# Kernel optimization log

Hardware: AMD Instinct MI355X
Metric: run time of the kernel (lower is better)

## Reference

```python
import jax, jax.numpy as jnp
import numpy as np

N, E, B, L = 65536, 262144, 512, 1000
IN_DIM, HID, VOCAB = 74, 128, 25
CHANNELS = [HID, 96, 128, IN_DIM, HID]  # protein conv1d filter chain


def _conv1d(x, k):
    # x: [B, C_in, L], k: [C_out, C_in, 3], stride 1, padding 1 (like nn.Conv1d)
    return jax.lax.conv_general_dilated(x, k, (1,), ((1, 1),),
                                        dimension_numbers=('NCH', 'OIH', 'NCH'))


def setup_inputs() -> dict:
    key = jax.random.key(0)
    ks = jax.random.split(key, 20)

    def gl(k, shape, fan_in):
        return jax.random.normal(k, shape, jnp.float32) / np.float32(np.sqrt(fan_in))

    inp = {}
    inp['node_feats'] = jax.random.normal(ks[0], (N, IN_DIM), jnp.float32)
    # GraphConv (conv1): weight [in, hid]
    inp['W_gc'] = gl(ks[1], (IN_DIM, HID), IN_DIM)
    inp['b_gc'] = jnp.zeros((HID,), jnp.float32)
    # MLPNodeReadout: two linears (no activation between, per dgllife default)
    inp['W_ro_in'] = gl(ks[2], (HID, HID), HID)
    inp['b_ro_in'] = jnp.zeros((HID,), jnp.float32)
    inp['W_ro_out'] = gl(ks[3], (HID, HID), HID)
    inp['b_ro_out'] = jnp.zeros((HID,), jnp.float32)
    inp['Wc1'] = gl(ks[4], (HID, HID), HID); inp['bc1'] = jnp.zeros((HID,), jnp.float32)
    inp['Wc2'] = gl(ks[5], (HID, HID), HID); inp['bc2'] = jnp.zeros((HID,), jnp.float32)
    # protein embedding + 4 conv1d layers
    inp['embed'] = jax.random.normal(ks[6], (VOCAB, HID), jnp.float32)
    for i in range(4):
        cin, cout = CHANNELS[i], CHANNELS[i + 1]
        inp['K%d' % (i + 1)] = gl(ks[7 + i], (cout, cin, 3), cin * 3)
        inp['cb%d' % (i + 1)] = jnp.zeros((cout,), jnp.float32)
    # CPI head: Linear(2h,2h)+ReLU, Linear(2h,1)+Sigmoid
    inp['Wf1'] = gl(ks[11], (2 * HID, 2 * HID), 2 * HID); inp['bf1'] = jnp.zeros((2 * HID,), jnp.float32)
    inp['Wf2'] = gl(ks[12], (2 * HID, 1), 2 * HID); inp['bf2'] = jnp.zeros((1,), jnp.float32)
    # graph structure / protein tokens
    inp['edge_src'] = jax.random.randint(ks[13], (E,), 0, N, jnp.int32)
    inp['edge_dst'] = jax.random.randint(ks[14], (E,), 0, N, jnp.int32)
    inp['graph_ids'] = jnp.sort(jax.random.randint(ks[15], (N,), 0, B, jnp.int32))
    inp['protein_seq'] = jax.random.randint(ks[16], (B, L), 0, VOCAB, jnp.int32)
    return inp


def reference(node_feats, W_gc, b_gc, W_ro_in, b_ro_in, W_ro_out, b_ro_out,
              Wc1, bc1, Wc2, bc2, embed, K1, cb1, K2, cb2, K3, cb3, K4, cb4,
              Wf1, bf1, Wf2, bf2, edge_src, edge_dst, graph_ids, protein_seq):
    n = node_feats.shape[0]
    nb = protein_seq.shape[0]
    # dgl.add_self_loop: append self edges
    loop = jnp.arange(n, dtype=edge_src.dtype)
    src = jnp.concatenate([edge_src, loop])
    dst = jnp.concatenate([edge_dst, loop])
    ones = jnp.ones(src.shape[0], jnp.float32)
    deg_out = jax.ops.segment_sum(ones, src, n)  # out-degree (src norm)
    deg_in = jax.ops.segment_sum(ones, dst, n)   # in-degree (dst norm)
    h = node_feats * jax.lax.rsqrt(deg_out)[:, None]
    h = jax.ops.segment_sum(h[src], dst, n) * jax.lax.rsqrt(deg_in)[:, None]
    h = jax.nn.relu(h @ W_gc + b_gc)
    # MLPNodeReadout (sum over nodes per graph), then outer ReLU
    x = (h @ W_ro_in + b_ro_in) @ W_ro_out + b_ro_out
    hg = jax.nn.relu(jax.ops.segment_sum(x, graph_ids, nb))  # [B, HID]
    # compound FC layers (dropout = identity)
    cv = jax.nn.relu(hg @ Wc1 + bc1)
    cv = jax.nn.relu(cv @ Wc2 + bc2)
    pv = jnp.transpose(embed[protein_seq], (0, 2, 1))
    for K, b in ((K1, cb1), (K2, cb2), (K3, cb3), (K4, cb4)):
        pv = jax.nn.relu(_conv1d(pv, K) + b[None, :, None])
    pmax = jnp.max(pv, axis=-1)  # adaptive_max_pool1d(output_size=1) + squeeze
    # CPI head
    z = jnp.concatenate([cv, pmax], axis=1)  # [B, 2*HID]
    z = jax.nn.relu(z @ Wf1 + bf1)
    return jax.nn.sigmoid(z @ Wf2 + bf2)  # [B, 1]
```

## Files before the change

kernel.cpp:

```cpp
#include <hip/hip_runtime.h>
#include <math.h>

#define IN_DIM 74
#define HID 128
#define LSEQ 1000
#define RSA 272
#define RSB 208
#define TILE 50
#define R0 58
#define R1 56
#define R2 54
#define R3 52
#define NCHUNK 42
#define NGRP 14
#define WBUF_SZ 24576
#define LDS_BIAS 49152
#define LDS_ACT  50944
#define ACTA_SZ  15776
#define ACTB_SZ  11648
#define ACTB_BASE (LDS_ACT + 4*ACTA_SZ)
#define LDS_TOTAL (ACTB_BASE + 4*ACTB_SZ)

typedef unsigned int u32;
typedef unsigned short u16;

typedef __attribute__((ext_vector_type(8))) short bf16x8;
typedef __attribute__((ext_vector_type(4))) float f32x4;

__device__ __forceinline__ u16 f2bf(float f){
  u32 u = __float_as_uint(f);
  u32 r = (u + 0x7fffu + ((u >> 16) & 1u)) >> 16;
  return (u16)r;
}
__device__ __forceinline__ u32 pack2(float x, float y){
  return (u32)f2bf(x) | ((u32)f2bf(y) << 16);
}

__global__ void k_cnt_edge(const int* __restrict__ src, const int* __restrict__ dst,
                           int* out_cnt, int* in_cnt, int E){
  int e = blockIdx.x*256 + threadIdx.x;
  if (e < E){ atomicAdd(&out_cnt[src[e]], 1); atomicAdd(&in_cnt[dst[e]], 1); }
}
__global__ void k_scan1(const int* __restrict__ cnt, int* pref, int* bsum, int N){
  __shared__ int buf[256];
  int t = threadIdx.x, i = blockIdx.x*256 + t;
  int v = (i < N) ? cnt[i] : 0;
  buf[t] = v; __syncthreads();
  for (int o = 1; o < 256; o <<= 1){
    int tv = (t >= o) ? buf[t-o] : 0;
    __syncthreads(); buf[t] += tv; __syncthreads();
  }
  if (i < N) pref[i] = buf[t] - v;
  if (t == 255) bsum[blockIdx.x] = buf[255];
}
__global__ void k_scan2(int* bsum, int nb){
  __shared__ int buf[1024];
  int t = threadIdx.x;
  int v = (t < nb) ? bsum[t] : 0;
  buf[t] = v; __syncthreads();
  for (int o = 1; o < 1024; o <<= 1){
    int tv = (t >= o) ? buf[t-o] : 0;
    __syncthreads(); buf[t] += tv; __syncthreads();
  }
  if (t < nb) bsum[t] = buf[t] - v;
}
__global__ void k_scan3(const int* __restrict__ pref, const int* __restrict__ bsum,
                        int* offs, int* cur, int N){
  int i = blockIdx.x*256 + threadIdx.x;
  if (i < N){ int o = pref[i] + bsum[blockIdx.x]; offs[i] = o; cur[i] = o; }
}
__global__ void k_csr_fill(const int* __restrict__ src, const int* __restrict__ dst,
                           int* cur, int* csr_src, int E){
  int e = blockIdx.x*256 + threadIdx.x;
  if (e < E){ int slot = atomicAdd(&cur[dst[e]], 1); csr_src[slot] = src[e]; }
}
__global__ __launch_bounds__(256) void k_gather(const float* __restrict__ nf,
    const int* __restrict__ csr_src, const int* __restrict__ offs,
    const int* __restrict__ in_cnt, const int* __restrict__ out_cnt,
    float* __restrict__ h_agg, int N){
  int wid = threadIdx.x >> 6, lane = threadIdx.x & 63;
  int d = blockIdx.x*4 + wid;
  if (d >= N) return;
  int beg = offs[d], num = in_cnt[d];
  const float* row = nf + (size_t)d*IN_DIM;
  float ws = rsqrtf((float)out_cnt[d] + 1.f);
  float a0 = row[lane]*ws, a1 = 0.f;
  if (lane < IN_DIM-64) a1 = row[64+lane]*ws;
  for (int j = 0; j < num; ++j){
    int s = csr_src[beg + j];
    float w = rsqrtf((float)out_cnt[s] + 1.f);
    const float* rs = nf + (size_t)s*IN_DIM;
    a0 += rs[lane]*w;
    if (lane < IN_DIM-64) a1 += rs[64+lane]*w;
  }
  float sc = rsqrtf((float)num + 1.f);
  float* hp = h_agg + (size_t)d*IN_DIM;
  hp[lane] = a0*sc;
  if (lane < IN_DIM-64) hp[64+lane] = a1*sc;
}
__global__ __launch_bounds__(256) void k_gc_gemm(const float* __restrict__ h_agg,
        const float* __restrict__ W, const float* __restrict__ bias,
        float* __restrict__ h, int N){
  __shared__ float Wl[IN_DIM*HID];
  __shared__ float rowsT[IN_DIM][36];
  int base = blockIdx.x * 32;
  for (int idx = threadIdx.x; idx < IN_DIM*HID; idx += 256) Wl[idx] = W[idx];
  for (int idx = threadIdx.x; idx < 32*IN_DIM; idx += 256){
    int r = idx / IN_DIM, k = idx - r*IN_DIM;
    rowsT[k][r] = (base + r < N) ? h_agg[(size_t)(base+r)*IN_DIM + k] : 0.f;
  }
  __syncthreads();
  int c = threadIdx.x & 127, rh = threadIdx.x >> 7;
  float acc[16];
  #pragma unroll
  for (int i = 0; i < 16; ++i) acc[i] = 0.f;
  for (int k = 0; k < IN_DIM; ++k){
    float w = Wl[k*HID + c];
    const float4* rp = (const float4*)&rowsT[k][rh*16];
    float4 r0 = rp[0], r1 = rp[1], r2 = rp[2], r3 = rp[3];
    acc[0] += r0.x*w; acc[1] += r0.y*w; acc[2] += r0.z*w; acc[3] += r0.w*w;
    acc[4] += r1.x*w; acc[5] += r1.y*w; acc[6] += r1.z*w; acc[7] += r1.w*w;
    acc[8] += r2.x*w; acc[9] += r2.y*w; acc[10] += r2.z*w; acc[11] += r2.w*w;
    acc[12] += r3.x*w; acc[13] += r3.y*w; acc[14] += r3.z*w; acc[15] += r3.w*w;
  }
  float bv = bias[c];
  #pragma unroll
  for (int i = 0; i < 16; ++i){
    int r = base + rh*16 + i;
    if (r < N) h[(size_t)r*HID + c] = fmaxf(acc[i] + bv, 0.f);
  }
}
__global__ __launch_bounds__(128) void k_graph_tail(const float* __restrict__ h,
    const int* __restrict__ gid,
    const float* __restrict__ W_ri, const float* __restrict__ b_ri,
    const float* __restrict__ W_ro, const float* __restrict__ b_ro,
    const float* __restrict__ Wc1, const float* __restrict__ bc1,
    const float* __restrict__ Wc2, const float* __restrict__ bc2,
    float* __restrict__ z, int N){
  __shared__ float va[128], vb[128];
  __shared__ int bounds[2];
  int g = blockIdx.x, c = threadIdx.x;
  if (c < 2){
    int target = g + c, lo = 0, hi = N;
    while (lo < hi){ int mid = (lo+hi)>>1; if (gid[mid] < target) lo = mid+1; else hi = mid; }
    bounds[c] = lo;
  }
  __syncthreads();
  int lo = bounds[0], hi = bounds[1];
  float s = 0.f;
  for (int i = lo; i < hi; ++i) s += h[(size_t)i*HID + c];
  va[c] = s;
  float cn = (float)(hi - lo);
  __syncthreads();
  s = 0.f;
  for (int k = 0; k < 128; ++k) s += va[k]*W_ri[k*128 + c];
  vb[c] = s + b_ri[c]*cn;
  __syncthreads();
  s = 0.f;
  for (int k = 0; k < 128; ++k) s += vb[k]*W_ro[k*128 + c];
  va[c] = fmaxf(s + b_ro[c]*cn, 0.f);
  __syncthreads();
  s = 0.f;
  for (int k = 0; k < 128; ++k) s += va[k]*Wc1[k*128 + c];
  vb[c] = fmaxf(s + bc1[c], 0.f);
  __syncthreads();
  s = 0.f;
  for (int k = 0; k < 128; ++k) s += vb[k]*Wc2[k*128 + c];
  z[(size_t)g*256 + c] = fmaxf(s + bc2[c], 0.f);
}

__global__ void k_setup(const float* __restrict__ K1, const float* __restrict__ K2,
                        const float* __restrict__ K3, const float* __restrict__ K4,
                        const float* __restrict__ cb1, const float* __restrict__ cb2,
                        const float* __restrict__ cb3, const float* __restrict__ cb4,
                        u16* __restrict__ AW, float* __restrict__ ball,
                        float* __restrict__ z, int* __restrict__ out_cnt,
                        int* __restrict__ in_cnt, int N, int B){
  int idx = blockIdx.x*256 + threadIdx.x;
  if (idx < NCHUNK*4096){
    int g = idx >> 12, rem = idx & 4095;
    int co = rem >> 5, kk = rem & 31;
    const float* Kw; int CIN, CPAD, COUT, ksl;
    if (g < 12)      { Kw = K1; CIN = 128; CPAD = 128; COUT =  96; ksl = g; }
    else if (g < 21) { Kw = K2; CIN =  96; CPAD =  96; COUT = 128; ksl = g-12; }
    else if (g < 33) { Kw = K3; CIN =  74; CPAD = 128; COUT =  74; ksl = g-21; }
    else             { Kw = K4; CIN =  74; CPAD =  96; COUT = 128; ksl = g-33; }
    int k = ksl*32 + kk;
    int t = k / CPAD, ci = k - t*CPAD;
    float v = (co < COUT && ci < CIN) ? Kw[((size_t)co*CIN + ci)*3 + t] : 0.f;
    int sl2 = (kk >> 3) ^ ((co >> 1) & 3);
    AW[(size_t)g*4096 + co*32 + sl2*8 + (kk & 7)] = f2bf(v);
    return;
  }
  idx -= NCHUNK*4096;
  if (idx < 448){
    float v = 0.f;
    if (idx < 96) v = cb1[idx];
    else if (idx < 224) v = cb2[idx-96];
    else if (idx < 320){ int c = idx-224; v = (c < 74) ? cb3[c] : 0.f; }
    else v = cb4[idx-320];
    ball[idx] = v;
    return;
  }
  idx -= 448;
  if (idx < B*128){ z[(size_t)(idx>>7)*256 + 128 + (idx&127)] = 0.f; return; }
  idx -= B*128;
  if (idx < 2*N){
    if (idx < N) out_cnt[idx] = 0; else in_cnt[idx-N] = 0;
  }
}

__device__ __forceinline__ void stage24k(char* lds, int tid, const u16* src, int pbuf){
  const char* s = (const char*)src;
  char* d = lds + pbuf*WBUF_SZ;
  #pragma unroll
  for (int i = 0; i < 3; ++i)
    __builtin_amdgcn_global_load_lds(
      (const __attribute__((address_space(1))) unsigned*)(s + i*8192 + tid*16),
      (__attribute__((address_space(3))) unsigned*)(d + i*8192 + tid*16), 16, 0, 0);
}

template<int KS, int G0, int M, int TPC, int RS_IN, int RCAP>
__device__ __forceinline__ void conv_phases(char* lds, const char* actIn,
    const u16* __restrict__ AW, int co0, int lm, int cg, int scg, int tid,
    f32x4 (&acc)[M][4])
{
  #pragma unroll
  for (int m = 0; m < M; ++m)
    #pragma unroll
    for (int n = 0; n < 4; ++n) acc[m][n] = (f32x4){0.f,0.f,0.f,0.f};
  #pragma unroll
  for (int ks = 0; ks < KS; ++ks){
    const int g = G0 + ks;
    const char* wb = lds + ((g/3)&1)*WBUF_SZ + (g%3)*8192;
    bf16x8 Af[M];
    #pragma unroll
    for (int m = 0; m < M; ++m)
      Af[m] = *(const bf16x8*)(wb + (co0 + m*16 + lm)*64 + scg*16);
    const int tap = ks / TPC;
    const int c16 = (ks - tap*TPC)*4 + cg;
    bf16x8 Bf[4];
    #pragma unroll
    for (int n = 0; n < 4; ++n){
      int raw = n*16 + lm + tap;
      int row = raw < RCAP ? raw : RCAP;
      Bf[n] = *(const bf16x8*)(actIn + row*RS_IN + c16*16);
    }
    __builtin_amdgcn_s_setprio(1);
    #pragma unroll
    for (int m = 0; m < M; ++m)
      #pragma unroll
      for (int n = 0; n < 4; ++n)
        acc[m][n] = __builtin_amdgcn_mfma_f32_16x16x32_bf16(Af[m], Bf[n], acc[m][n], 0, 0, 0);
    __builtin_amdgcn_s_setprio(0);
    if ((g % 3) == 2 && (ks + 1 < KS)){
      __syncthreads();
      const int gn = g/3 + 2;
      if (gn < NGRP) stage24k(lds, tid, AW + (size_t)gn*12288, gn & 1);
    }
  }
}

template<int M>
__device__ __forceinline__ void epi_store(char* actOut, int RS_OUT,
    const float* lbias, int boff, int co0, int lm, int cg,
    int lbase, int nrows, f32x4 (&acc)[M][4])
{
  #pragma unroll
  for (int m = 0; m < M; ++m){
    int co = co0 + m*16 + cg*4;
    float4 bb = *(const float4*)(lbias + boff + co);
    #pragma unroll
    for (int n = 0; n < 4; ++n){
      int r1 = n*16 + lm;
      if (r1 < nrows){
        int l = lbase + r1;
        u32 lo = 0, hi = 0;
        if ((unsigned)l < (unsigned)LSEQ){
          f32x4 a = acc[m][n];
          lo = pack2(fmaxf(a[0]+bb.x, 0.f), fmaxf(a[1]+bb.y, 0.f));
          hi = pack2(fmaxf(a[2]+bb.z, 0.f), fmaxf(a[3]+bb.w, 0.f));
        }
        uint2 st; st.x = lo; st.y = hi;
        *(uint2*)(actOut + r1*RS_OUT + co*2) = st;
      }
    }
  }
}

__device__ __forceinline__ void epi_pool(const float* lbias, int boff,
    int co0, int lm, int cg, int l0, float* __restrict__ z, int b, f32x4 (&acc)[4][4])
{
  float mxv[4][4];
  #pragma unroll
  for (int m = 0; m < 4; ++m)
    #pragma unroll
    for (int j = 0; j < 4; ++j) mxv[m][j] = 0.f;
  #pragma unroll
  for (int m = 0; m < 4; ++m){
    float4 bb = *(const float4*)(lbias + boff + co0 + m*16 + cg*4);
    const float* bv = (const float*)&bb;
    #pragma unroll
    for (int n = 0; n < 4; ++n){
      int r1 = n*16 + lm;
      int l = l0 + r1;
      if (r1 < TILE && l < LSEQ){
        #pragma unroll
        for (int j = 0; j < 4; ++j)
          mxv[m][j] = fmaxf(mxv[m][j], fmaxf(acc[m][n][j] + bv[j], 0.f));
      }
    }
  }
  #pragma unroll
  for (int o = 1; o <= 8; o <<= 1)
    #pragma unroll
    for (int m = 0; m < 4; ++m)
      #pragma unroll
      for (int j = 0; j < 4; ++j)
        mxv[m][j] = fmaxf(mxv[m][j], __shfl_xor(mxv[m][j], o));
  if (lm == 0){
    float* zrow = z + (size_t)b*256 + 128;
    #pragma unroll
    for (int m = 0; m < 4; ++m)
      #pragma unroll
      for (int j = 0; j < 4; ++j)
        atomicMax((u32*)(zrow + co0 + m*16 + cg*4 + j), __float_as_uint(mxv[m][j]));
  }
}

__global__ __launch_bounds__(512, 1) void k_protein(
    const int* __restrict__ seq, const float* __restrict__ emb,
    const u16* __restrict__ AW, const float* __restrict__ ball,
    float* __restrict__ z)
{
  __shared__ __align__(16) char lds[LDS_TOTAL];
  const int tid = threadIdx.x;
  const int lane = tid & 63, wid = tid >> 6;
  const int lm = lane & 15, cg = lane >> 4;
  const int scg = cg ^ ((lm >> 1) & 3);
  const int tl = wid >> 1;
  const int h  = wid & 1;
  const int b  = blockIdx.y;
  const int l0 = (blockIdx.x*4 + tl) * TILE;

  for (int i = tid; i < 448; i += 512) ((float*)(lds + LDS_BIAS))[i] = ball[i];

  for (int idx = tid; idx < 4*R0*16; idx += 512){
    int t2 = idx / (R0*16), rem = idx - t2*(R0*16);
    int r = rem >> 4, p = rem & 15;
    int ll0 = (blockIdx.x*4 + t2) * TILE;
    int l = ll0 - 4 + r;
    uint4 st = make_uint4(0u,0u,0u,0u);
    if ((unsigned)l < (unsigned)LSEQ){
      int tok = seq[b*LSEQ + l];
      const float4* e = (const float4*)(emb + (size_t)tok*HID + p*8);
      float4 v0 = e[0], v1 = e[1];
      st.x = pack2(v0.x, v0.y); st.y = pack2(v0.z, v0.w);
      st.z = pack2(v1.x, v1.y); st.w = pack2(v1.z, v1.w);
    }
    *(uint4*)(lds + LDS_ACT + t2*ACTA_SZ + r*RSA + p*16) = st;
  }
  stage24k(lds, tid, AW, 0);
  stage24k(lds, tid, AW + 12288, 1);
  __syncthreads();

  char* actA = lds + LDS_ACT + tl*ACTA_SZ;
  char* actB = lds + ACTB_BASE + tl*ACTB_SZ;
  const float* lbias = (const float*)(lds + LDS_BIAS);

  {
    f32x4 acc[3][4];
    conv_phases<12,0,3,4,RSA,R0-1>(lds, actA, AW, h*48, lm, cg, scg, tid, acc);
    epi_store<3>(actB, RSB, lbias, 0, h*48, lm, cg, l0-3, R1, acc);
    __syncthreads();
    stage24k(lds, tid, AW + (size_t)5*12288, 5 & 1);
  }
  {
    f32x4 acc[4][4];
    conv_phases<9,12,4,3,RSB,R1-1>(lds, actB, AW, h*64, lm, cg, scg, tid, acc);
    epi_store<4>(actA, RSA, lbias, 96, h*64, lm, cg, l0-2, R2, acc);
    __syncthreads();
    stage24k(lds, tid, AW + (size_t)8*12288, 8 & 1);
  }
  {
    f32x4 acc[3][4];
    conv_phases<12,21,3,4,RSA,R2-1>(lds, actA, AW, h*48, lm, cg, scg, tid, acc);
    epi_store<3>(actB, RSB, lbias, 224, h*48, lm, cg, l0-1, R3, acc);
    __syncthreads();
    stage24k(lds, tid, AW + (size_t)12*12288, 12 & 1);
  }
  {
    f32x4 acc[4][4];
    conv_phases<9,33,4,3,RSB,R3-1>(lds, actB, AW, h*64, lm, cg, scg, tid, acc);
    epi_pool(lbias, 320, h*64, lm, cg, l0, z, b, acc);
  }
}

__global__ __launch_bounds__(256) void k_fc_head(const float* __restrict__ z,
    const float* __restrict__ Wf1, const float* __restrict__ bf1,
    const float* __restrict__ Wf2, const float* __restrict__ bf2v,
    float* __restrict__ out){
  __shared__ float za[256];
  __shared__ float red[4];
  int r = blockIdx.x, c = threadIdx.x;
  za[c] = z[(size_t)r*256 + c];
  __syncthreads();
  float s = 0.f;
  for (int k = 0; k < 256; ++k) s += za[k]*Wf1[(size_t)k*256 + c];
  s = fmaxf(s + bf1[c], 0.f);
  float p = s * Wf2[c];
  for (int o = 32; o; o >>= 1) p += __shfl_xor(p, o);
  if ((c & 63) == 0) red[c >> 6] = p;
  __syncthreads();
  if (c == 0) out[r] = 1.f/(1.f + __expf(-(red[0]+red[1]+red[2]+red[3] + bf2v[0])));
}

extern "C" void kernel_launch(void* const* d_in, const int* in_sizes, int n_in,
                              void* d_out, int out_size, void* d_ws, size_t ws_size,
                              hipStream_t stream){
  const float* nf   = (const float*)d_in[0];
  const float* W_gc = (const float*)d_in[1];
  const float* b_gc = (const float*)d_in[2];
  const float* W_ri = (const float*)d_in[3];
  const float* b_ri = (const float*)d_in[4];
  const float* W_ro = (const float*)d_in[5];
  const float* b_ro = (const float*)d_in[6];
  const float* Wc1  = (const float*)d_in[7];
  const float* bc1  = (const float*)d_in[8];
  const float* Wc2  = (const float*)d_in[9];
  const float* bc2  = (const float*)d_in[10];
  const float* emb  = (const float*)d_in[11];
  const float* K1 = (const float*)d_in[12]; const float* cb1 = (const float*)d_in[13];
  const float* K2 = (const float*)d_in[14]; const float* cb2 = (const float*)d_in[15];
  const float* K3 = (const float*)d_in[16]; const float* cb3 = (const float*)d_in[17];
  const float* K4 = (const float*)d_in[18]; const float* cb4 = (const float*)d_in[19];
  const float* Wf1 = (const float*)d_in[20]; const float* bf1 = (const float*)d_in[21];
  const float* Wf2 = (const float*)d_in[22]; const float* bf2v = (const float*)d_in[23];
  const int* esrc = (const int*)d_in[24];
  const int* edst = (const int*)d_in[25];
  const int* gids = (const int*)d_in[26];
  const int* seq  = (const int*)d_in[27];
  float* out = (float*)d_out;

  int N = in_sizes[26];
  int E = in_sizes[24];
  int B = out_size;
  int nb = (N + 255)/256;

  char* ws = (char*)d_ws;
  size_t off = 0;
  auto take = [&](size_t bytes)->char*{
    char* p = ws + off; off = (off + bytes + 255) & ~(size_t)255; return p;
  };
  float* z      = (float*)take((size_t)B*2*HID*4);
  int* out_cnt  = (int*)take((size_t)N*4);
  int* in_cnt   = (int*)take((size_t)N*4);
  int* pref     = (int*)take((size_t)N*4);
  int* offs     = (int*)take((size_t)N*4);
  int* cur      = (int*)take((size_t)N*4);
  int* bsum     = (int*)take(1024*4);
  int* csr_src  = (int*)take((size_t)E*4);
  u16* AW       = (u16*)take((size_t)NCHUNK*8192);
  float* ball   = (float*)take(448*4);
  float* h_agg  = (float*)take((size_t)N*IN_DIM*4);
  float* h      = (float*)take((size_t)N*HID*4);

  int setup_total = NCHUNK*4096 + 448 + B*128 + 2*N;
  k_setup<<<(setup_total+255)/256, 256, 0, stream>>>(K1, K2, K3, K4, cb1, cb2, cb3, cb4,
                                                     AW, ball, z, out_cnt, in_cnt, N, B);

  k_cnt_edge<<<(E+255)/256, 256, 0, stream>>>(esrc, edst, out_cnt, in_cnt, E);
  k_scan1<<<nb, 256, 0, stream>>>(in_cnt, pref, bsum, N);
  k_scan2<<<1, 1024, 0, stream>>>(bsum, nb);
  k_scan3<<<nb, 256, 0, stream>>>(pref, bsum, offs, cur, N);
  k_csr_fill<<<(E+255)/256, 256, 0, stream>>>(esrc, edst, cur, csr_src, E);
  k_gather<<<(N+3)/4, 256, 0, stream>>>(nf, csr_src, offs, in_cnt, out_cnt, h_agg, N);
  k_gc_gemm<<<(N+31)/32, 256, 0, stream>>>(h_agg, W_gc, b_gc, h, N);
  k_graph_tail<<<B, 128, 0, stream>>>(h, gids, W_ri, b_ri, W_ro, b_ro,
                                      Wc1, bc1, Wc2, bc2, z, N);

  dim3 pgrid(5, B);
  k_protein<<<pgrid, 512, 0, stream>>>(seq, emb, AW, ball, z);

  k_fc_head<<<B, 256, 0, stream>>>(z, Wf1, bf1, Wf2, bf2v, out);
}
```

Measured before the change: 423.4 us.

## Fuse gather, GraphConv GEMM and per-graph segment sum into one kernel

The CSR neighbor gather, the GraphConv GEMM with ReLU, and the per-graph node sum are merged into a single kernel. Each block gathers 32 aggregated rows straight into shared memory, runs the GEMM, and atomically adds run-length partial sums per graph id into a small [B,HID] buffer. This removes the h_agg and h intermediate arrays (about 50 MB of writes and re-reads) and the serial per-graph reduction loop in k_graph_tail. In exchange it adds float atomics, which make the summation order nondeterministic, and it puts the gather latency in front of the GEMM within each block.

```diff
diff --git a/kernel.cpp b/kernel.cpp
--- a/kernel.cpp
+++ b/kernel.cpp
@@ -74,43 +74,46 @@
   int e = blockIdx.x*256 + threadIdx.x;
   if (e < E){ int slot = atomicAdd(&cur[dst[e]], 1); csr_src[slot] = src[e]; }
 }
-__global__ __launch_bounds__(256) void k_gather(const float* __restrict__ nf,
+
+__global__ __launch_bounds__(256) void k_mega(const float* __restrict__ nf,
     const int* __restrict__ csr_src, const int* __restrict__ offs,
     const int* __restrict__ in_cnt, const int* __restrict__ out_cnt,
-    float* __restrict__ h_agg, int N){
-  int wid = threadIdx.x >> 6, lane = threadIdx.x & 63;
-  int d = blockIdx.x*4 + wid;
-  if (d >= N) return;
-  int beg = offs[d], num = in_cnt[d];
-  const float* row = nf + (size_t)d*IN_DIM;
-  float ws = rsqrtf((float)out_cnt[d] + 1.f);
-  float a0 = row[lane]*ws, a1 = 0.f;
-  if (lane < IN_DIM-64) a1 = row[64+lane]*ws;
-  for (int j = 0; j < num; ++j){
-    int s = csr_src[beg + j];
-    float w = rsqrtf((float)out_cnt[s] + 1.f);
-    const float* rs = nf + (size_t)s*IN_DIM;
-    a0 += rs[lane]*w;
-    if (lane < IN_DIM-64) a1 += rs[64+lane]*w;
-  }
-  float sc = rsqrtf((float)num + 1.f);
-  float* hp = h_agg + (size_t)d*IN_DIM;
-  hp[lane] = a0*sc;
-  if (lane < IN_DIM-64) hp[64+lane] = a1*sc;
-}
-__global__ __launch_bounds__(256) void k_gc_gemm(const float* __restrict__ h_agg,
-        const float* __restrict__ W, const float* __restrict__ bias,
-        float* __restrict__ h, int N){
+    const float* __restrict__ W, const float* __restrict__ bias,
+    const int* __restrict__ gid, float* __restrict__ S, int N){
   __shared__ float Wl[IN_DIM*HID];
   __shared__ float rowsT[IN_DIM][36];
-  int base = blockIdx.x * 32;
-  for (int idx = threadIdx.x; idx < IN_DIM*HID; idx += 256) Wl[idx] = W[idx];
-  for (int idx = threadIdx.x; idx < 32*IN_DIM; idx += 256){
-    int r = idx / IN_DIM, k = idx - r*IN_DIM;
-    rowsT[k][r] = (base + r < N) ? h_agg[(size_t)(base+r)*IN_DIM + k] : 0.f;
-  }
-  __syncthreads();
-  int c = threadIdx.x & 127, rh = threadIdx.x >> 7;
+  __shared__ int lgid[32];
+  const int tid = threadIdx.x;
+  const int base = blockIdx.x * 32;
+  for (int i = tid; i < IN_DIM*HID; i += 256) Wl[i] = W[i];
+  if (tid < 32) lgid[tid] = (base + tid < N) ? gid[base + tid] : 0;
+
+  int wid = tid >> 6, lane = tid & 63;
+  for (int nn = wid; nn < 32; nn += 4){
+    int d = base + nn;
+    float a0 = 0.f, a1 = 0.f;
+    if (d < N){
+      int beg = offs[d], num = in_cnt[d];
+      const float* row = nf + (size_t)d*IN_DIM;
+      float ws = rsqrtf((float)out_cnt[d] + 1.f);
+      a0 = row[lane]*ws;
+      if (lane < IN_DIM-64) a1 = row[64+lane]*ws;
+      for (int j = 0; j < num; ++j){
+        int s = csr_src[beg + j];
+        float w = rsqrtf((float)out_cnt[s] + 1.f);
+        const float* rs = nf + (size_t)s*IN_DIM;
+        a0 += rs[lane]*w;
+        if (lane < IN_DIM-64) a1 += rs[64+lane]*w;
+      }
+      float sc = rsqrtf((float)num + 1.f);
+      a0 *= sc; a1 *= sc;
+    }
+    rowsT[lane][nn] = a0;
+    if (lane < IN_DIM-64) rowsT[64+lane][nn] = a1;
+  }
+  __syncthreads();
+
+  int c = tid & 127, rh = tid >> 7;
   float acc[16];
   #pragma unroll
   for (int i = 0; i < 16; ++i) acc[i] = 0.f;
@@ -124,13 +127,23 @@
     acc[12] += r3.x*w; acc[13] += r3.y*w; acc[14] += r3.z*w; acc[15] += r3.w*w;
   }
   float bv = bias[c];
+  float run = 0.f;
+  int curg = lgid[rh*16];
   #pragma unroll
   for (int i = 0; i < 16; ++i){
-    int r = base + rh*16 + i;
-    if (r < N) h[(size_t)r*HID + c] = fmaxf(acc[i] + bv, 0.f);
-  }
-}
-__global__ __launch_bounds__(128) void k_graph_tail(const float* __restrict__ h,
+    int node = rh*16 + i;
+    if (base + node >= N) break;
+    int g = lgid[node];
+    if (g != curg){
+      if (run != 0.f) atomicAdd(&S[(size_t)curg*HID + c], run);
+      run = 0.f; curg = g;
+    }
+    run += fmaxf(acc[i] + bv, 0.f);
+  }
+  if (run != 0.f) atomicAdd(&S[(size_t)curg*HID + c], run);
+}
+
+__global__ __launch_bounds__(128) void k_graph_tail(const float* __restrict__ S,
     const int* __restrict__ gid,
     const float* __restrict__ W_ri, const float* __restrict__ b_ri,
     const float* __restrict__ W_ro, const float* __restrict__ b_ro,
@@ -146,13 +159,10 @@
     bounds[c] = lo;
   }
   __syncthreads();
-  int lo = bounds[0], hi = bounds[1];
+  float cn = (float)(bounds[1] - bounds[0]);
+  va[c] = S[(size_t)g*HID + c];
+  __syncthreads();
   float s = 0.f;
-  for (int i = lo; i < hi; ++i) s += h[(size_t)i*HID + c];
-  va[c] = s;
-  float cn = (float)(hi - lo);
-  __syncthreads();
-  s = 0.f;
   for (int k = 0; k < 128; ++k) s += va[k]*W_ri[k*128 + c];
   vb[c] = s + b_ri[c]*cn;
   __syncthreads();
@@ -174,8 +184,9 @@
                         const float* __restrict__ cb1, const float* __restrict__ cb2,
                         const float* __restrict__ cb3, const float* __restrict__ cb4,
                         u16* __restrict__ AW, float* __restrict__ ball,
-                        float* __restrict__ z, int* __restrict__ out_cnt,
-                        int* __restrict__ in_cnt, int N, int B){
+                        float* __restrict__ z, float* __restrict__ S,
+                        int* __restrict__ out_cnt, int* __restrict__ in_cnt,
+                        int N, int B){
   int idx = blockIdx.x*256 + threadIdx.x;
   if (idx < NCHUNK*4096){
     int g = idx >> 12, rem = idx & 4095;
@@ -204,6 +215,8 @@
   }
   idx -= 448;
   if (idx < B*128){ z[(size_t)(idx>>7)*256 + 128 + (idx&127)] = 0.f; return; }
+  idx -= B*128;
+  if (idx < B*128){ S[idx] = 0.f; return; }
   idx -= B*128;
   if (idx < 2*N){
     if (idx < N) out_cnt[idx] = 0; else in_cnt[idx-N] = 0;
@@ -453,6 +466,7 @@
     char* p = ws + off; off = (off + bytes + 255) & ~(size_t)255; return p;
   };
   float* z      = (float*)take((size_t)B*2*HID*4);
+  float* S      = (float*)take((size_t)B*HID*4);
   int* out_cnt  = (int*)take((size_t)N*4);
   int* in_cnt   = (int*)take((size_t)N*4);
   int* pref     = (int*)take((size_t)N*4);
@@ -462,21 +476,19 @@
   int* csr_src  = (int*)take((size_t)E*4);
   u16* AW       = (u16*)take((size_t)NCHUNK*8192);
   float* ball   = (float*)take(448*4);
-  float* h_agg  = (float*)take((size_t)N*IN_DIM*4);
-  float* h      = (float*)take((size_t)N*HID*4);
-
-  int setup_total = NCHUNK*4096 + 448 + B*128 + 2*N;
+
+  int setup_total = NCHUNK*4096 + 448 + B*128 + B*128 + 2*N;
   k_setup<<<(setup_total+255)/256, 256, 0, stream>>>(K1, K2, K3, K4, cb1, cb2, cb3, cb4,
-                                                     AW, ball, z, out_cnt, in_cnt, N, B);
+                                                     AW, ball, z, S, out_cnt, in_cnt, N, B);
 
   k_cnt_edge<<<(E+255)/256, 256, 0, stream>>>(esrc, edst, out_cnt, in_cnt, E);
   k_scan1<<<nb, 256, 0, stream>>>(in_cnt, pref, bsum, N);
   k_scan2<<<1, 1024, 0, stream>>>(bsum, nb);
   k_scan3<<<nb, 256, 0, stream>>>(pref, bsum, offs, cur, N);
   k_csr_fill<<<(E+255)/256, 256, 0, stream>>>(esrc, edst, cur, csr_src, E);
-  k_gather<<<(N+3)/4, 256, 0, stream>>>(nf, csr_src, offs, in_cnt, out_cnt, h_agg, N);
-  k_gc_gemm<<<(N+31)/32, 256, 0, stream>>>(h_agg, W_gc, b_gc, h, N);
-  k_graph_tail<<<B, 128, 0, stream>>>(h, gids, W_ri, b_ri, W_ro, b_ro,
+  k_mega<<<(N+31)/32, 256, 0, stream>>>(nf, csr_src, offs, in_cnt, out_cnt,
+                                        W_gc, b_gc, gids, S, N);
+  k_graph_tail<<<B, 128, 0, stream>>>(S, gids, W_ri, b_ri, W_ro, b_ro,
                                       Wc1, bc1, Wc2, bc2, z, N);
 
   dim3 pgrid(5, B);
```

After: 420.7 us. Within noise of the previous version (-0.6%).
